# Kernel tuning notes

Hardware: AMD Instinct MI355X
Metric: run time of the kernel (lower is better)

The kernel has to match this reference:

```python
import jax, jax.numpy as jnp
import numpy as np

N_EMBED = 1024
HEAD_SIZE = 128
B, T = 4, 4096

def setup_inputs() -> dict:
    key = jax.random.key(0)
    kx, kk, kq, kv = jax.random.split(key, 4)
    s = (1.0 / np.sqrt(N_EMBED)).astype(np.float32)
    return {
        "x": jax.random.normal(kx, (B, T, N_EMBED), dtype=jnp.float32),
        "W_key": jax.random.normal(kk, (N_EMBED, HEAD_SIZE), dtype=jnp.float32) * s,
        "W_query": jax.random.normal(kq, (N_EMBED, HEAD_SIZE), dtype=jnp.float32) * s,
        "W_value": jax.random.normal(kv, (N_EMBED, HEAD_SIZE), dtype=jnp.float32) * s,
    }

def reference(x, W_key, W_query, W_value):
    # x: [B,T,C]; single-head causal attention. NOTE: scale is C**-0.5 (n_embed),
    # matching the original source (not head_size**-0.5).
    Bn, Tn, C = x.shape
    k = jnp.einsum('btc,cd->btd', x, W_key)    # [B,T,d]
    q = jnp.einsum('btc,cd->btd', x, W_query)  # [B,T,d]
    v = jnp.einsum('btc,cd->btd', x, W_value)  # [B,T,d]
    scores = jnp.einsum('btd,bsd->bts', q, k) * (C ** -0.5)  # [B,T,T]
    causal = jnp.tril(jnp.ones((Tn, Tn), dtype=bool))
    scores = jnp.where(causal[None, :, :], scores, -jnp.inf)
    attn = jax.nn.softmax(scores, axis=-1)
    return jnp.einsum('bts,bsd->btd', attn, v)
```

## Files before the change

kernel.cpp:

```cpp
#include <hip/hip_runtime.h>
#include <hip/hip_bf16.h>

typedef __attribute__((ext_vector_type(8))) short bf16x8;
typedef __attribute__((ext_vector_type(4))) float f32x4;
typedef __attribute__((ext_vector_type(4))) unsigned short us4;

__device__ __forceinline__ unsigned short f2bf(float f) {
    union { float f; unsigned u; } c; c.f = f;
    unsigned u = c.u;
    u += 0x7fffu + ((u >> 16) & 1u);
    return (unsigned short)(u >> 16);
}
__device__ __forceinline__ float bf2f(unsigned short h) {
    union { unsigned u; float f; } c; c.u = ((unsigned)h) << 16;
    return c.f;
}
__device__ __forceinline__ unsigned cvt_pk_bf16(float lo, float hi) {
    unsigned r;
    asm volatile("v_cvt_pk_bf16_f32 %0, %1, %2" : "=v"(r) : "v"(lo), "v"(hi));
    return r;
}
__device__ __forceinline__ void gload_lds16(const void* g, void* l) {
    __builtin_amdgcn_global_load_lds(
        (const __attribute__((address_space(1))) unsigned int*)g,
        (__attribute__((address_space(3))) unsigned int*)l, 16, 0, 0);
}

#define QSCALE 0.04508422f

__global__ __launch_bounds__(256) void wconv_kernel(
        const float* __restrict__ Wk, const float* __restrict__ Wq,
        const float* __restrict__ Wv, unsigned short* __restrict__ WbT) {
    int idx = blockIdx.x * 256 + threadIdx.x;
    int n = idx >> 10, kk = idx & 1023;
    const float* W = (n < 128) ? Wk : (n < 256) ? Wq : Wv;
    int col = n & 127;
    WbT[idx] = f2bf(W[kk * 128 + col]);
}

__global__ __launch_bounds__(512) void qkv_gemm_kernel(
        const float* __restrict__ x, const unsigned short* __restrict__ WbT,
        unsigned short* __restrict__ kw, unsigned short* __restrict__ qw,
        unsigned short* __restrict__ vTw) {
    __shared__ __align__(16) unsigned short Bl[2][192 * 64];
    __shared__ __align__(16) unsigned short Al[2][64 * 72];
    const int tid = threadIdx.x;
    const int m0 = (blockIdx.x >> 1) * 64;
    const int nb = blockIdx.x & 1;
    const int w = tid >> 6, l = tid & 63;
    const int l15 = l & 15, lh = l >> 4;
    const int wm = w >> 2, wn = w & 3;

    f32x4 acc[2][3] = {};

    const int srcsw = ((((l & 7) * 16) ^ ((l >> 3) << 4)) >> 1);
    const unsigned short* gB[3];
    #pragma unroll
    for (int it = 0; it < 3; ++it)
        gB[it] = WbT + (size_t)(nb * 192 + it * 64 + w * 8 + (l >> 3)) * 1024 + srcsw;

    const float* xr = &x[(size_t)(m0 + (tid >> 3)) * 1024 + (tid & 7) * 8];
    const int aoff = (tid >> 3) * 72 + (tid & 7) * 8;

    #define STAGE_B(buf, k0) do { \
        _Pragma("unroll") \
        for (int it = 0; it < 3; ++it) \
            gload_lds16(gB[it] + (k0), &Bl[buf][(it * 64 + w * 8) * 64]); \
    } while (0)

    STAGE_B(0, 0);
    {
        float4 a0 = *(const float4*)(xr);
        float4 a1 = *(const float4*)(xr + 4);
        uint4 pk;
        pk.x = cvt_pk_bf16(a0.x, a0.y); pk.y = cvt_pk_bf16(a0.z, a0.w);
        pk.z = cvt_pk_bf16(a1.x, a1.y); pk.w = cvt_pk_bf16(a1.z, a1.w);
        *(uint4*)&Al[0][aoff] = pk;
    }
    __syncthreads();

    int cur = 0;
    for (int t = 0; t < 16; ++t) {
        float4 a0, a1;
        const bool more = (t + 1 < 16);
        if (more) {
            STAGE_B(cur ^ 1, (t + 1) * 64);
            a0 = *(const float4*)(xr + (t + 1) * 64);
            a1 = *(const float4*)(xr + (t + 1) * 64 + 4);
        }
        const unsigned short* Bc = Bl[cur];
        const unsigned short* Ac = Al[cur];
        for (int kc = 0; kc < 2; ++kc) {
            bf16x8 a[2], bb[3];
            for (int mi = 0; mi < 2; ++mi)
                a[mi] = *(const bf16x8*)&Ac[(wm * 32 + mi * 16 + l15) * 72 + kc * 32 + lh * 8];
            for (int ni = 0; ni < 3; ++ni) {
                int n = wn * 48 + ni * 16 + l15;
                bb[ni] = *(const bf16x8*)((const char*)Bc + n * 128 +
                        ((kc * 64 + lh * 16) ^ ((n & 7) << 4)));
            }
            for (int mi = 0; mi < 2; ++mi)
                for (int ni = 0; ni < 3; ++ni)
                    acc[mi][ni] = __builtin_amdgcn_mfma_f32_16x16x32_bf16(
                            a[mi], bb[ni], acc[mi][ni], 0, 0, 0);
        }
        if (more) {
            uint4 pk;
            pk.x = cvt_pk_bf16(a0.x, a0.y); pk.y = cvt_pk_bf16(a0.z, a0.w);
            pk.z = cvt_pk_bf16(a1.x, a1.y); pk.w = cvt_pk_bf16(a1.z, a1.w);
            *(uint4*)&Al[cur ^ 1][aoff] = pk;
        }
        __syncthreads();
        cur ^= 1;
    }
    #undef STAGE_B

    for (int mi = 0; mi < 2; ++mi)
        for (int ni = 0; ni < 3; ++ni) {
            int col = nb * 192 + wn * 48 + ni * 16 + l15;
            int sect = col >> 7, cc = col & 127;
            if (sect < 2) {
                unsigned short* dst = (sect == 0) ? kw : qw;
                float fs = (sect == 0) ? 1.0f : QSCALE;
                for (int i = 0; i < 4; ++i) {
                    int row = m0 + wm * 32 + mi * 16 + lh * 4 + i;
                    dst[(size_t)row * 128 + cc] = f2bf(acc[mi][ni][i] * fs);
                }
            } else {
                int trow0 = m0 + wm * 32 + mi * 16 + lh * 4;
                int b = trow0 >> 12, t0 = trow0 & 4095;
                union { unsigned short u[4]; us4 v; } pk;
                for (int i = 0; i < 4; ++i) pk.u[i] = f2bf(acc[mi][ni][i]);
                *(us4*)&vTw[((size_t)(b * 128 + cc)) * 4096 + t0] = pk.v;
            }
        }
}

__global__ __launch_bounds__(512, 2) void attn_kernel(
        const unsigned short* __restrict__ kw, const unsigned short* __restrict__ qw,
        const unsigned short* __restrict__ vTw,
        unsigned short* __restrict__ pO, float* __restrict__ pL,
        int nCPB, int G, int TPC) {
    __shared__ __align__(16) unsigned short Kl[64 * 128];
    __shared__ __align__(16) unsigned short Vl[128 * 64];
    __shared__ __align__(16) unsigned short Pl[8][1024];

    const int tid = threadIdx.x;
    const int wgid = blockIdx.x;
    const int xcd = wgid & 7, slot = wgid >> 3;
    const int b = xcd >> 1, half = xcd & 1;
    const int cid = (nCPB - 1) - (slot * 2 + half);
    const int halfG = G >> 1;
    int a = 0;
    while (halfG * (a + 1) * (a + 2) <= cid) ++a;
    int rem = cid - halfG * a * (a + 1);
    const int g = G * a + rem / (a + 1);
    const int c = rem % (a + 1);
    const int kt0 = c * TPC;
    const int kt1 = min(kt0 + TPC, 2 * g + 2);

    const int w = tid >> 6, l = tid & 63;
    const int l15 = l & 15, lh = l >> 4;
    const int qrow0 = g * 128 + w * 16;

    bf16x8 qa[4];
    {
        size_t grow = (size_t)b * 4096 + qrow0 + l15;
        for (int cc = 0; cc < 4; ++cc)
            qa[cc] = *(const bf16x8*)&qw[grow * 128 + cc * 32 + lh * 8];
    }
    bf16x8 ones;
    for (int u = 0; u < 8; ++u) ones[u] = (short)0x3F80;

    f32x4 o[8] = {};
    f32x4 lsa = {0.f, 0.f, 0.f, 0.f};

    const int kr_ = tid >> 3;
    const int vd_ = tid >> 2;
    bf16x8 kReg[2], vReg[2];
    auto issue = [&](int kt) {
        int kv0 = kt * 64;
        const unsigned short* ks = &kw[((size_t)(b * 4096 + kv0 + kr_)) * 128 + (tid & 7) * 16];
        kReg[0] = *(const bf16x8*)ks;
        kReg[1] = *(const bf16x8*)(ks + 8);
        const unsigned short* vs = &vTw[((size_t)(b * 128 + vd_)) * 4096 + kv0 + (tid & 3) * 16];
        vReg[0] = *(const bf16x8*)vs;
        vReg[1] = *(const bf16x8*)(vs + 8);
    };

    char* Plw = (char*)&Pl[w][0];

    issue(kt0);
    for (int kt = kt0; kt < kt1; ++kt) {
        __syncthreads();
        for (int it = 0; it < 2; ++it)
            *(bf16x8*)((char*)Kl + kr_ * 256 +
                    (((tid & 7) * 32 + it * 16) ^ ((kr_ & 7) << 4))) = kReg[it];
        for (int it = 0; it < 2; ++it)
            *(bf16x8*)((char*)Vl + vd_ * 128 +
                    (((tid & 3) * 32 + it * 16) ^ ((vd_ & 7) << 4))) = vReg[it];
        __syncthreads();
        if (kt + 1 < kt1) issue(kt + 1);

        const int kv0 = kt * 64;
        if (kv0 > qrow0 + 15) continue;

        f32x4 s[4];
        __builtin_amdgcn_s_setprio(1);
        for (int ni = 0; ni < 4; ++ni) {
            s[ni] = (f32x4){0.f, 0.f, 0.f, 0.f};
            int kr = ni * 16 + l15;
            int sw = (kr & 7) << 4;
            for (int cc = 0; cc < 4; ++cc) {
                bf16x8 bk = *(bf16x8*)((char*)Kl + kr * 256 + ((lh * 16 + cc * 64) ^ sw));
                s[ni] = __builtin_amdgcn_mfma_f32_16x16x32_bf16(bk, qa[cc], s[ni], 0, 0, 0);
            }
        }
        __builtin_amdgcn_s_setprio(0);

        if (kv0 + 63 > qrow0) {
            int qg = qrow0 + l15;
            for (int ni = 0; ni < 4; ++ni)
                for (int i = 0; i < 4; ++i)
                    if (kv0 + ni * 16 + lh * 4 + i > qg) s[ni][i] = -INFINITY;
        }
        for (int ni = 0; ni < 4; ++ni) {
            float p0 = exp2f(s[ni][0]), p1 = exp2f(s[ni][1]);
            float p2 = exp2f(s[ni][2]), p3 = exp2f(s[ni][3]);
            uint2 pk;
            pk.x = cvt_pk_bf16(p0, p1);
            pk.y = cvt_pk_bf16(p2, p3);
            *(uint2*)(Plw + l15 * 128 + ((ni * 32 + lh * 8) ^ ((l15 & 7) << 4))) = pk;
        }
        bf16x8 pa[2];
        for (int kc = 0; kc < 2; ++kc)
            pa[kc] = *(bf16x8*)(Plw + l15 * 128 +
                    ((kc * 64 + lh * 16) ^ ((l15 & 7) << 4)));
        __builtin_amdgcn_s_setprio(1);
        lsa = __builtin_amdgcn_mfma_f32_16x16x32_bf16(pa[1], ones,
              __builtin_amdgcn_mfma_f32_16x16x32_bf16(pa[0], ones, lsa, 0, 0, 0), 0, 0, 0);
        for (int nd = 0; nd < 8; ++nd) {
            int dr = nd * 16 + l15;
            int sw = (dr & 7) << 4;
            for (int kc = 0; kc < 2; ++kc) {
                bf16x8 bv = *(bf16x8*)((char*)Vl + dr * 128 + ((lh * 16 + kc * 64) ^ sw));
                o[nd] = __builtin_amdgcn_mfma_f32_16x16x32_bf16(pa[kc], bv, o[nd], 0, 0, 0);
            }
        }
        __builtin_amdgcn_s_setprio(0);
    }

    const int slot_ = b * nCPB + cid;
    unsigned short* po = pO + (size_t)slot_ * 16384;
    for (int nd = 0; nd < 8; ++nd)
        for (int i = 0; i < 4; ++i)
            po[(w * 16 + lh * 4 + i) * 128 + nd * 16 + l15] = f2bf(o[nd][i]);
    if (l15 == 0) {
        float* pl = pL + (size_t)slot_ * 128;
        for (int i = 0; i < 4; ++i)
            pl[w * 16 + lh * 4 + i] = lsa[i];
    }
}

__global__ __launch_bounds__(256) void combine_kernel(
        const unsigned short* __restrict__ pO, const float* __restrict__ pL,
        float* __restrict__ out, int nCPB, int G) {
    int idx = blockIdx.x * 256 + threadIdx.x;
    int row = idx >> 4, d8 = (idx & 15) * 8;
    int b = row >> 12, t = row & 4095;
    int g = t >> 7, rowin = t & 127;
    int a = g / G;
    int nch = a + 1;
    int base = b * nCPB + (G >> 1) * a * (a + 1) + (g - G * a) * (a + 1);

    float den = 0.f;
    float num[8] = {0.f, 0.f, 0.f, 0.f, 0.f, 0.f, 0.f, 0.f};
    for (int cc = 0; cc < nch; ++cc) {
        den += pL[(size_t)(base + cc) * 128 + rowin];
        bf16x8 ov = *(const bf16x8*)&pO[(size_t)(base + cc) * 16384 + rowin * 128 + d8];
        for (int u = 0; u < 8; ++u)
            num[u] += bf2f((unsigned short)ov[u]);
    }
    float inv = 1.f / den;
    for (int u = 0; u < 8; ++u)
        out[(size_t)row * 128 + d8 + u] = num[u] * inv;
}

extern "C" void kernel_launch(void* const* d_in, const int* in_sizes, int n_in,
                              void* d_out, int out_size, void* d_ws, size_t ws_size,
                              hipStream_t stream) {
    const float* x  = (const float*)d_in[0];
    const float* Wk = (const float*)d_in[1];
    const float* Wq = (const float*)d_in[2];
    const float* Wv = (const float*)d_in[3];
    float* out = (float*)d_out;

    char* ws = (char*)d_ws;
    unsigned short* WbT = (unsigned short*)(ws);
    unsigned short* kw  = (unsigned short*)(ws + 786432);
    unsigned short* qw  = (unsigned short*)(ws + 786432 + 4194304);
    unsigned short* vTw = (unsigned short*)(ws + 786432 + 2 * 4194304);
    size_t base = 786432 + 3 * (size_t)4194304;

    int nCPB, G, TPC;
    size_t need4 = base + (size_t)1088 * 32768 + (size_t)1088 * 512;
    if (ws_size >= need4) { nCPB = 272; G = 2; TPC = 4; }
    else                  { nCPB = 144; G = 4; TPC = 8; }
    int nslots = 4 * nCPB;
    unsigned short* pO = (unsigned short*)(ws + base);
    float*          pL = (float*)(ws + base + (size_t)nslots * 32768);

    wconv_kernel<<<1536, 256, 0, stream>>>(Wk, Wq, Wv, WbT);
    qkv_gemm_kernel<<<512, 512, 0, stream>>>(x, WbT, kw, qw, vTw);
    attn_kernel<<<nslots, 512, 0, stream>>>(kw, qw, vTw, pO, pL, nCPB, G, TPC);
    combine_kernel<<<1024, 256, 0, stream>>>(pO, pL, out, nCPB, G);
}
```

Measured before the change: 82.26 us.

## Double-buffer K/V via direct global-to-LDS loads and restructure projection pipeline

The attention kernel now stages K and V tiles straight into double-buffered LDS with global_load_lds, pre-swizzling the source addresses. This replaces the register round-trip and cuts the per-tile barriers from two to one. The projection GEMM loop is unrolled by two with fixed buffer indices, A prefetch two steps ahead, and explicit vmcnt-based barriers so fewer loads are forced to complete at each sync. The cost is doubled LDS for K/V, and the dropped occupancy hint in launch_bounds may lower waves per CU.

```diff
diff --git a/kernel.cpp b/kernel.cpp
--- a/kernel.cpp
+++ b/kernel.cpp
@@ -62,58 +62,70 @@
     const float* xr = &x[(size_t)(m0 + (tid >> 3)) * 1024 + (tid & 7) * 8];
     const int aoff = (tid >> 3) * 72 + (tid & 7) * 8;
 
-    #define STAGE_B(buf, k0) do { \
+    float4 aE0, aE1, aO0, aO1;
+
+    #define STAGE_B(buf, t_) do { \
         _Pragma("unroll") \
         for (int it = 0; it < 3; ++it) \
-            gload_lds16(gB[it] + (k0), &Bl[buf][(it * 64 + w * 8) * 64]); \
+            gload_lds16(gB[it] + (t_) * 64, &Bl[buf][(it * 64 + w * 8) * 64]); \
     } while (0)
+    #define ISSUE_A(d0, d1, t_) do { \
+        d0 = *(const float4*)(xr + (t_) * 64); \
+        d1 = *(const float4*)(xr + (t_) * 64 + 4); } while (0)
+    #define WRITE_A(buf, s0, s1) do { \
+        uint4 pk_; \
+        pk_.x = cvt_pk_bf16(s0.x, s0.y); pk_.y = cvt_pk_bf16(s0.z, s0.w); \
+        pk_.z = cvt_pk_bf16(s1.x, s1.y); pk_.w = cvt_pk_bf16(s1.z, s1.w); \
+        *(uint4*)&Al[buf][aoff] = pk_; } while (0)
+    #define MFMA_ON(buf) do { \
+        for (int kc = 0; kc < 2; ++kc) { \
+            bf16x8 a_[2], bb_[3]; \
+            for (int mi = 0; mi < 2; ++mi) \
+                a_[mi] = *(const bf16x8*)&Al[buf][(wm * 32 + mi * 16 + l15) * 72 + kc * 32 + lh * 8]; \
+            for (int ni = 0; ni < 3; ++ni) { \
+                int n_ = wn * 48 + ni * 16 + l15; \
+                bb_[ni] = *(const bf16x8*)((const char*)Bl[buf] + n_ * 128 + \
+                        ((kc * 64 + lh * 16) ^ ((n_ & 7) << 4))); \
+            } \
+            for (int mi = 0; mi < 2; ++mi) \
+                for (int ni = 0; ni < 3; ++ni) \
+                    acc[mi][ni] = __builtin_amdgcn_mfma_f32_16x16x32_bf16( \
+                            a_[mi], bb_[ni], acc[mi][ni], 0, 0, 0); \
+        } } while (0)
+    #define BAR(n_) do { \
+        asm volatile("s_waitcnt vmcnt(" #n_ ") lgkmcnt(0)" ::: "memory"); \
+        __builtin_amdgcn_sched_barrier(0); \
+        __builtin_amdgcn_s_barrier(); } while (0)
 
     STAGE_B(0, 0);
-    {
-        float4 a0 = *(const float4*)(xr);
-        float4 a1 = *(const float4*)(xr + 4);
-        uint4 pk;
-        pk.x = cvt_pk_bf16(a0.x, a0.y); pk.y = cvt_pk_bf16(a0.z, a0.w);
-        pk.z = cvt_pk_bf16(a1.x, a1.y); pk.w = cvt_pk_bf16(a1.z, a1.w);
-        *(uint4*)&Al[0][aoff] = pk;
-    }
-    __syncthreads();
-
-    int cur = 0;
-    for (int t = 0; t < 16; ++t) {
-        float4 a0, a1;
-        const bool more = (t + 1 < 16);
-        if (more) {
-            STAGE_B(cur ^ 1, (t + 1) * 64);
-            a0 = *(const float4*)(xr + (t + 1) * 64);
-            a1 = *(const float4*)(xr + (t + 1) * 64 + 4);
+    ISSUE_A(aE0, aE1, 0);
+    ISSUE_A(aO0, aO1, 1);
+    WRITE_A(0, aE0, aE1);
+    BAR(2);
+
+    #pragma unroll 1
+    for (int tt = 0; tt < 8; ++tt) {
+        const int t0 = tt * 2;
+        STAGE_B(1, t0 + 1);
+        if (t0 + 2 < 16) ISSUE_A(aE0, aE1, t0 + 2);
+        MFMA_ON(0);
+        WRITE_A(1, aO0, aO1);
+        if (t0 + 2 < 16) BAR(2); else BAR(0);
+        if (t0 + 2 < 16) {
+            STAGE_B(0, t0 + 2);
+            if (t0 + 3 < 16) ISSUE_A(aO0, aO1, t0 + 3);
+            MFMA_ON(1);
+            WRITE_A(0, aE0, aE1);
+            if (t0 + 3 < 16) BAR(2); else BAR(0);
+        } else {
+            MFMA_ON(1);
         }
-        const unsigned short* Bc = Bl[cur];
-        const unsigned short* Ac = Al[cur];
-        for (int kc = 0; kc < 2; ++kc) {
-            bf16x8 a[2], bb[3];
-            for (int mi = 0; mi < 2; ++mi)
-                a[mi] = *(const bf16x8*)&Ac[(wm * 32 + mi * 16 + l15) * 72 + kc * 32 + lh * 8];
-            for (int ni = 0; ni < 3; ++ni) {
-                int n = wn * 48 + ni * 16 + l15;
-                bb[ni] = *(const bf16x8*)((const char*)Bc + n * 128 +
-                        ((kc * 64 + lh * 16) ^ ((n & 7) << 4)));
-            }
-            for (int mi = 0; mi < 2; ++mi)
-                for (int ni = 0; ni < 3; ++ni)
-                    acc[mi][ni] = __builtin_amdgcn_mfma_f32_16x16x32_bf16(
-                            a[mi], bb[ni], acc[mi][ni], 0, 0, 0);
-        }
-        if (more) {
-            uint4 pk;
-            pk.x = cvt_pk_bf16(a0.x, a0.y); pk.y = cvt_pk_bf16(a0.z, a0.w);
-            pk.z = cvt_pk_bf16(a1.x, a1.y); pk.w = cvt_pk_bf16(a1.z, a1.w);
-            *(uint4*)&Al[cur ^ 1][aoff] = pk;
-        }
-        __syncthreads();
-        cur ^= 1;
     }
     #undef STAGE_B
+    #undef ISSUE_A
+    #undef WRITE_A
+    #undef MFMA_ON
+    #undef BAR
 
     for (int mi = 0; mi < 2; ++mi)
         for (int ni = 0; ni < 3; ++ni) {
@@ -128,21 +140,21 @@
                 }
             } else {
                 int trow0 = m0 + wm * 32 + mi * 16 + lh * 4;
-                int b = trow0 >> 12, t0 = trow0 & 4095;
+                int b = trow0 >> 12, t0_ = trow0 & 4095;
                 union { unsigned short u[4]; us4 v; } pk;
                 for (int i = 0; i < 4; ++i) pk.u[i] = f2bf(acc[mi][ni][i]);
-                *(us4*)&vTw[((size_t)(b * 128 + cc)) * 4096 + t0] = pk.v;
+                *(us4*)&vTw[((size_t)(b * 128 + cc)) * 4096 + t0_] = pk.v;
             }
         }
 }
 
-__global__ __launch_bounds__(512, 2) void attn_kernel(
+__global__ __launch_bounds__(512) void attn_kernel(
         const unsigned short* __restrict__ kw, const unsigned short* __restrict__ qw,
         const unsigned short* __restrict__ vTw,
         unsigned short* __restrict__ pO, float* __restrict__ pL,
         int nCPB, int G, int TPC) {
-    __shared__ __align__(16) unsigned short Kl[64 * 128];
-    __shared__ __align__(16) unsigned short Vl[128 * 64];
+    __shared__ __align__(16) unsigned short Kl[2][64 * 128];
+    __shared__ __align__(16) unsigned short Vl[2][128 * 64];
     __shared__ __align__(16) unsigned short Pl[8][1024];
 
     const int tid = threadIdx.x;
@@ -175,80 +187,84 @@
     f32x4 o[8] = {};
     f32x4 lsa = {0.f, 0.f, 0.f, 0.f};
 
-    const int kr_ = tid >> 3;
-    const int vd_ = tid >> 2;
-    bf16x8 kReg[2], vReg[2];
-    auto issue = [&](int kt) {
-        int kv0 = kt * 64;
-        const unsigned short* ks = &kw[((size_t)(b * 4096 + kv0 + kr_)) * 128 + (tid & 7) * 16];
-        kReg[0] = *(const bf16x8*)ks;
-        kReg[1] = *(const bf16x8*)(ks + 8);
-        const unsigned short* vs = &vTw[((size_t)(b * 128 + vd_)) * 4096 + kv0 + (tid & 3) * 16];
-        vReg[0] = *(const bf16x8*)vs;
-        vReg[1] = *(const bf16x8*)(vs + 8);
-    };
+    const int kc0 = 2 * w, kc1 = 2 * w + 1;
+    const int kr0 = 4 * kc0 + (l >> 4), kr1 = 4 * kc1 + (l >> 4);
+    const unsigned short* gk0 = kw + ((size_t)(b * 4096 + kr0)) * 128 +
+            (((((l & 15) * 16) ^ ((kr0 & 7) << 4))) >> 1);
+    const unsigned short* gk1 = kw + ((size_t)(b * 4096 + kr1)) * 128 +
+            (((((l & 15) * 16) ^ ((kr1 & 7) << 4))) >> 1);
+    const int vd0 = 8 * kc0 + (l >> 3), vd1 = 8 * kc1 + (l >> 3);
+    const unsigned short* gv0 = vTw + ((size_t)(b * 128 + vd0)) * 4096 +
+            (((((l & 7) * 16) ^ ((vd0 & 7) << 4))) >> 1);
+    const unsigned short* gv1 = vTw + ((size_t)(b * 128 + vd1)) * 4096 +
+            (((((l & 7) * 16) ^ ((vd1 & 7) << 4))) >> 1);
+
+    #define STAGE(B_, kt_) do { \
+        int kv_ = (kt_) * 64; \
+        gload_lds16(gk0 + (size_t)kv_ * 128, &Kl[B_][kc0 * 512]); \
+        gload_lds16(gk1 + (size_t)kv_ * 128, &Kl[B_][kc1 * 512]); \
+        gload_lds16(gv0 + kv_, &Vl[B_][kc0 * 512]); \
+        gload_lds16(gv1 + kv_, &Vl[B_][kc1 * 512]); } while (0)
 
     char* Plw = (char*)&Pl[w][0];
 
-    issue(kt0);
+    STAGE(0, kt0);
+    __syncthreads();
+    int cur = 0;
     for (int kt = kt0; kt < kt1; ++kt) {
+        if (kt + 1 < kt1) STAGE(cur ^ 1, kt + 1);
+        const int kv0 = kt * 64;
+        if (kv0 <= qrow0 + 15) {
+            const char* Kc = (const char*)Kl[cur];
+            const char* Vc = (const char*)Vl[cur];
+            f32x4 s[4];
+            __builtin_amdgcn_s_setprio(1);
+            for (int ni = 0; ni < 4; ++ni) {
+                s[ni] = (f32x4){0.f, 0.f, 0.f, 0.f};
+                int kr = ni * 16 + l15;
+                int sw = (kr & 7) << 4;
+                for (int cc = 0; cc < 4; ++cc) {
+                    bf16x8 bk = *(bf16x8*)(Kc + kr * 256 + ((lh * 16 + cc * 64) ^ sw));
+                    s[ni] = __builtin_amdgcn_mfma_f32_16x16x32_bf16(bk, qa[cc], s[ni], 0, 0, 0);
+                }
+            }
+            __builtin_amdgcn_s_setprio(0);
+
+            if (kv0 + 63 > qrow0) {
+                int qg = qrow0 + l15;
+                for (int ni = 0; ni < 4; ++ni)
+                    for (int i = 0; i < 4; ++i)
+                        if (kv0 + ni * 16 + lh * 4 + i > qg) s[ni][i] = -INFINITY;
+            }
+            for (int ni = 0; ni < 4; ++ni) {
+                float p0 = exp2f(s[ni][0]), p1 = exp2f(s[ni][1]);
+                float p2 = exp2f(s[ni][2]), p3 = exp2f(s[ni][3]);
+                uint2 pk;
+                pk.x = cvt_pk_bf16(p0, p1);
+                pk.y = cvt_pk_bf16(p2, p3);
+                *(uint2*)(Plw + l15 * 128 + ((ni * 32 + lh * 8) ^ ((l15 & 7) << 4))) = pk;
+            }
+            bf16x8 pa[2];
+            for (int kc = 0; kc < 2; ++kc)
+                pa[kc] = *(bf16x8*)(Plw + l15 * 128 +
+                        ((kc * 64 + lh * 16) ^ ((l15 & 7) << 4)));
+            __builtin_amdgcn_s_setprio(1);
+            lsa = __builtin_amdgcn_mfma_f32_16x16x32_bf16(pa[1], ones,
+                  __builtin_amdgcn_mfma_f32_16x16x32_bf16(pa[0], ones, lsa, 0, 0, 0), 0, 0, 0);
+            for (int nd = 0; nd < 8; ++nd) {
+                int dr = nd * 16 + l15;
+                int sw = (dr & 7) << 4;
+                for (int kc = 0; kc < 2; ++kc) {
+                    bf16x8 bv = *(bf16x8*)(Vc + dr * 128 + ((lh * 16 + kc * 64) ^ sw));
+                    o[nd] = __builtin_amdgcn_mfma_f32_16x16x32_bf16(pa[kc], bv, o[nd], 0, 0, 0);
+                }
+            }
+            __builtin_amdgcn_s_setprio(0);
+        }
         __syncthreads();
-        for (int it = 0; it < 2; ++it)
-            *(bf16x8*)((char*)Kl + kr_ * 256 +
-                    (((tid & 7) * 32 + it * 16) ^ ((kr_ & 7) << 4))) = kReg[it];
-        for (int it = 0; it < 2; ++it)
-            *(bf16x8*)((char*)Vl + vd_ * 128 +
-                    (((tid & 3) * 32 + it * 16) ^ ((vd_ & 7) << 4))) = vReg[it];
-        __syncthreads();
-        if (kt + 1 < kt1) issue(kt + 1);
-
-        const int kv0 = kt * 64;
-        if (kv0 > qrow0 + 15) continue;
-
-        f32x4 s[4];
-        __builtin_amdgcn_s_setprio(1);
-        for (int ni = 0; ni < 4; ++ni) {
-            s[ni] = (f32x4){0.f, 0.f, 0.f, 0.f};
-            int kr = ni * 16 + l15;
-            int sw = (kr & 7) << 4;
-            for (int cc = 0; cc < 4; ++cc) {
-                bf16x8 bk = *(bf16x8*)((char*)Kl + kr * 256 + ((lh * 16 + cc * 64) ^ sw));
-                s[ni] = __builtin_amdgcn_mfma_f32_16x16x32_bf16(bk, qa[cc], s[ni], 0, 0, 0);
-            }
-        }
-        __builtin_amdgcn_s_setprio(0);
-
-        if (kv0 + 63 > qrow0) {
-            int qg = qrow0 + l15;
-            for (int ni = 0; ni < 4; ++ni)
-                for (int i = 0; i < 4; ++i)
-                    if (kv0 + ni * 16 + lh * 4 + i > qg) s[ni][i] = -INFINITY;
-        }
-        for (int ni = 0; ni < 4; ++ni) {
-            float p0 = exp2f(s[ni][0]), p1 = exp2f(s[ni][1]);
-            float p2 = exp2f(s[ni][2]), p3 = exp2f(s[ni][3]);
-            uint2 pk;
-            pk.x = cvt_pk_bf16(p0, p1);
-            pk.y = cvt_pk_bf16(p2, p3);
-            *(uint2*)(Plw + l15 * 128 + ((ni * 32 + lh * 8) ^ ((l15 & 7) << 4))) = pk;
-        }
-        bf16x8 pa[2];
-        for (int kc = 0; kc < 2; ++kc)
-            pa[kc] = *(bf16x8*)(Plw + l15 * 128 +
-                    ((kc * 64 + lh * 16) ^ ((l15 & 7) << 4)));
-        __builtin_amdgcn_s_setprio(1);
-        lsa = __builtin_amdgcn_mfma_f32_16x16x32_bf16(pa[1], ones,
-              __builtin_amdgcn_mfma_f32_16x16x32_bf16(pa[0], ones, lsa, 0, 0, 0), 0, 0, 0);
-        for (int nd = 0; nd < 8; ++nd) {
-            int dr = nd * 16 + l15;
-            int sw = (dr & 7) << 4;
-            for (int kc = 0; kc < 2; ++kc) {
-                bf16x8 bv = *(bf16x8*)((char*)Vl + dr * 128 + ((lh * 16 + kc * 64) ^ sw));
-                o[nd] = __builtin_amdgcn_mfma_f32_16x16x32_bf16(pa[kc], bv, o[nd], 0, 0, 0);
-            }
-        }
-        __builtin_amdgcn_s_setprio(0);
-    }
+        cur ^= 1;
+    }
+    #undef STAGE
 
     const int slot_ = b * nCPB + cid;
     unsigned short* po = pO + (size_t)slot_ * 16384;
```

New measurement: 81.79 us. No clear change (-0.6%).
